# Kernel tuning notes

Measured on AMD Instinct MI355X. Metric: run time of the kernel, lower is better.

The kernel has to match this reference:

```python
import jax, jax.numpy as jnp
import numpy as np

H, W, CIN, COUT, B = 56, 56, 64, 64, 32
K = 3            # kernel_size
WIN = 15         # win_range
R = (WIN - 1) // 2


def _make_sample_idx():
    """Per-pixel fixed random sample locations within a WINxWIN window,
    mirroring Dconv_drop.__init__ (random.sample over valid window indices)."""
    rng = np.random.default_rng(0)
    ii = np.arange(H)[:, None, None]          # [H,1,1]
    jj = np.arange(W)[None, :, None]          # [1,W,1]
    lo_i = np.maximum(0, ii - R); hi_i = np.minimum(H - 1, ii + R)
    lo_j = np.maximum(0, jj - R); hi_j = np.minimum(W - 1, jj + R)
    ri = rng.integers(np.broadcast_to(lo_i, (H, W, K * K)),
                      np.broadcast_to(hi_i, (H, W, K * K)) + 1)
    rj = rng.integers(np.broadcast_to(lo_j, (H, W, K * K)),
                      np.broadcast_to(hi_j, (H, W, K * K)) + 1)
    return (ri * W + rj).astype(np.int32)    # [H,W,9] indices into H*W


def setup_inputs() -> dict:
    key = jax.random.key(0)
    k1, k2 = jax.random.split(key)
    x = jax.random.normal(k1, (B, CIN, H, W), dtype=jnp.float32)
    weight = jax.random.normal(k2, (COUT, CIN, K, K), dtype=jnp.float32) * 0.05
    sample_idx = jnp.asarray(_make_sample_idx())
    return {"x": x, "weight": weight, "sample_idx": sample_idx}


def reference(x, weight, sample_idx):
    # x: [B,C,H,W]; sample_idx: [H,W,9] flat indices into H*W.
    # Original: scatter gathered pixels into [B,C,3H,3W] grid, then
    # stride-3 kernel-3 conv => per-pixel contraction over the 9 samples.
    b, c, h, w = x.shape
    x_flat = x.reshape(b, c, h * w)
    gathered = x_flat[:, :, sample_idx]              # [B,C,H,W,9]
    w_flat = weight.reshape(weight.shape[0], c, K * K)  # [O,C,9]
    out = jnp.einsum('bchwk,ock->bohw', gathered, w_flat)
    return out
```

## Files before the change

kernel.cpp:

```cpp
#include <hip/hip_runtime.h>
#include <hip/hip_bf16.h>

#define HH 56
#define WW 56
#define CIN 64
#define COUT 64
#define BATCH 32
#define KK 9
#define HWP (HH*WW)
#define NS 18
#define NTILE 49
#define NBLK (NTILE*BATCH)
#define XT_OFF 73728
#define XSW 33

typedef __attribute__((ext_vector_type(8))) short short8;
typedef __attribute__((ext_vector_type(4))) float float4v;
typedef __attribute__((ext_vector_type(4))) unsigned int uint4v;

__device__ __forceinline__ unsigned short f2bf(float f) {
    union { float f; unsigned u; } v; v.f = f;
    unsigned r = v.u + 0x7FFFu + ((v.u >> 16) & 1u);
    return (unsigned short)(r >> 16);
}

__device__ __forceinline__ void prepack_elem(const float* __restrict__ w,
                                             unsigned short* __restrict__ apack,
                                             int e) {
    int j = e & 7;
    int l = (e >> 3) & 63;
    int ss = e >> 9;
    int mb = ss / 18;
    int s  = ss - mb * 18;
    int o = mb * 16 + (l & 15);
    int c = ((s & 1) << 5) + ((l >> 4) << 3) + j;
    int k = s >> 1;
    apack[e] = f2bf(w[(o * CIN + c) * KK + k]);
}

__global__ __launch_bounds__(256) void prep_kernel(
    const float* __restrict__ x, const float* __restrict__ w,
    unsigned int* __restrict__ xt, unsigned short* __restrict__ apack)
{
    int bid = blockIdx.x;
    int t   = threadIdx.x;
    if (bid < 784) {
        int u   = bid * 256 + t;
        int c2q = u & 7;
        int hq  = u >> 3;
        int b   = hq / 784;
        int q   = hq - b * 784;
        int hw  = q * 4;
        const float* xb = x + ((size_t)b * CIN + c2q * 8) * HWP + hw;
        float4v f[8];
        #pragma unroll
        for (int i = 0; i < 8; ++i)
            f[i] = *(const float4v*)(xb + (size_t)i * HWP);
        unsigned int* xto = xt + ((size_t)b * HWP + hw) * 32 + c2q * 4;
        #pragma unroll
        for (int j = 0; j < 4; ++j) {
            uint4v o;
            #pragma unroll
            for (int ci = 0; ci < 4; ++ci)
                o[ci] = (unsigned)f2bf(f[2 * ci][j]) |
                        ((unsigned)f2bf(f[2 * ci + 1][j]) << 16);
            *(uint4v*)(xto + (size_t)j * 32) = o;
        }
    } else {
        prepack_elem(w, apack, (bid - 784) * 256 + t);
    }
}

__global__ __launch_bounds__(256) void prep_weights_only(
    const float* __restrict__ w, unsigned short* __restrict__ apack)
{
    prepack_elem(w, apack, blockIdx.x * 256 + threadIdx.x);
}

__global__ __launch_bounds__(256) void dconv_main(
    const unsigned int* __restrict__ xt, const int* __restrict__ sidx,
    const unsigned short* __restrict__ apack, float* __restrict__ out)
{
    __shared__ unsigned int xs[496 * 16];

    const int t    = threadIdx.x;
    const int lane = t & 63;
    const int wv   = t >> 6;
    const int mbp  = wv >> 1;
    const int ntp  = wv & 1;
    const int col  = lane & 15;
    const int krow = lane >> 4;

    int bid  = blockIdx.x;
    int orig = (bid & 7) * 196 + (bid >> 3);
    int b    = orig / NTILE;
    int bx   = orig - b * NTILE;
    int ti = bx / 7, tj = bx - (bx / 7) * 7;
    int r0 = ti * 8 - 7; if (r0 < 0) r0 = 0;
    int c0 = tj * 8 - 7; if (c0 < 0) c0 = 0;

    const unsigned int* xtb = xt + (size_t)b * HWP * 32;

    int lb[2][KK];
    #pragma unroll
    for (int nn = 0; nn < 2; ++nn) {
        int p  = (ntp * 2 + nn) * 16 + col;
        int gi = ti * 8 + (p >> 3), gj = tj * 8 + (p & 7);
        const int* sp = sidx + (gi * WW + gj) * KK;
        #pragma unroll
        for (int k = 0; k < KK; ++k) {
            int g  = sp[k];
            int si = g / WW, sj = g - si * WW;
            int row = (si - r0) * 22 + (sj - c0);
            lb[nn][k] = row * 64 + ((krow ^ (row & 3)) << 4);
        }
    }

    const unsigned short* apW = apack + (size_t)(mbp * 2 * NS) * 512 + lane * 8;

    float4v zero = {0.f, 0.f, 0.f, 0.f};
    float4v acc[2][2] = {{zero, zero}, {zero, zero}};
    const char* xsb = (const char*)xs;

    #pragma unroll
    for (int sh = 0; sh < 2; ++sh) {
        for (int grp = wv; grp < 31; grp += 4) {
            int row = grp * 16 + (lane >> 2);
            int rc  = row < 483 ? row : 483;
            int lsr = rc / 22;
            int lsc = rc - lsr * 22;
            int si = r0 + lsr; if (si > HH - 1) si = HH - 1;
            int sj = c0 + lsc; if (sj > WW - 1) sj = WW - 1;
            int q  = (lane & 3) ^ (rc & 3);
            const unsigned int* src =
                xtb + (size_t)(si * WW + sj) * 32 + sh * 16 + (q << 2);
            __builtin_amdgcn_global_load_lds(
                (const __attribute__((address_space(1))) unsigned int*)src,
                (__attribute__((address_space(3))) unsigned int*)(xs + grp * 256),
                16, 0, 0);
        }
        __syncthreads();

        #pragma unroll
        for (int k = 0; k < KK; ++k) {
            short8 a0 = *(const short8*)(apW + (size_t)(2 * k + sh) * 512);
            short8 a1 = *(const short8*)(apW + (size_t)(NS + 2 * k + sh) * 512);
            #pragma unroll
            for (int nn = 0; nn < 2; ++nn) {
                short8 bv = *(const short8*)(xsb + lb[nn][k]);
                acc[0][nn] = __builtin_amdgcn_mfma_f32_16x16x32_bf16(
                    a0, bv, acc[0][nn], 0, 0, 0);
                acc[1][nn] = __builtin_amdgcn_mfma_f32_16x16x32_bf16(
                    a1, bv, acc[1][nn], 0, 0, 0);
            }
        }
        if (sh == 0) __syncthreads();
    }

    float* ob = out + ((size_t)b * COUT + mbp * 32) * HWP;
    #pragma unroll
    for (int m = 0; m < 2; ++m) {
        #pragma unroll
        for (int nn = 0; nn < 2; ++nn) {
            int p = (ntp * 2 + nn) * 16 + col;
            int g = (ti * 8 + (p >> 3)) * WW + tj * 8 + (p & 7);
            #pragma unroll
            for (int r = 0; r < 4; ++r)
                ob[(m * 16 + krow * 4 + r) * HWP + g] = acc[m][nn][r];
        }
    }
}

__global__ __launch_bounds__(256, 2) void dconv_fb(
    const float* __restrict__ x, const int* __restrict__ sidx,
    const unsigned short* __restrict__ apack, float* __restrict__ out)
{
    __shared__ unsigned int xs[484 * XSW];

    const int t    = threadIdx.x;
    const int lane = t & 63;
    const int wv   = t >> 6;
    const int mbp  = wv >> 1;
    const int ntp  = wv & 1;
    const int col  = lane & 15;
    const int krow = lane >> 4;
    const int bx   = blockIdx.x;
    const int b    = blockIdx.y;
    const int ti = bx / 7, tj = bx - (bx / 7) * 7;
    int r0 = ti * 8 - 7; if (r0 < 0) r0 = 0;
    int r1 = ti * 8 + 14; if (r1 > HH - 1) r1 = HH - 1;
    int c0 = tj * 8 - 7; if (c0 < 0) c0 = 0;
    int c1 = tj * 8 + 14; if (c1 > WW - 1) c1 = WW - 1;

    int lb[2][KK];
    #pragma unroll
    for (int nn = 0; nn < 2; ++nn) {
        int p  = (ntp * 2 + nn) * 16 + col;
        int gi = ti * 8 + (p >> 3), gj = tj * 8 + (p & 7);
        const int* sp = sidx + (gi * WW + gj) * KK;
        #pragma unroll
        for (int k = 0; k < KK; ++k) {
            int g  = sp[k];
            int si = g / WW, sj = g - si * WW;
            lb[nn][k] = ((si - r0) * 22 + (sj - c0)) * (XSW * 4);
        }
    }

    short8 areg[2][NS];
    #pragma unroll
    for (int m = 0; m < 2; ++m) {
        const unsigned short* ap = apack + ((mbp * 2 + m) * NS) * 512 + lane * 8;
        #pragma unroll
        for (int s = 0; s < NS; ++s)
            areg[m][s] = *(const short8*)(ap + s * 512);
    }

    const float* xb = x + (size_t)b * CIN * HWP;
    for (int e = t; e < 32 * 512; e += 256) {
        int c2 = e >> 9, ls = e & 511;
        if (ls < 484) {
            int lsr = ls / 22;
            int si = r0 + lsr, sj = c0 + (ls - lsr * 22);
            if (si <= r1 && sj <= c1) {
                int g = si * WW + sj;
                float f0 = xb[(2 * c2) * HWP + g];
                float f1 = xb[(2 * c2 + 1) * HWP + g];
                xs[ls * XSW + c2] =
                    (unsigned)f2bf(f0) | ((unsigned)f2bf(f1) << 16);
            }
        }
    }
    __syncthreads();

    float4v zero = {0.f, 0.f, 0.f, 0.f};
    float4v acc[2][2] = {{zero, zero}, {zero, zero}};
    const char* xsb = (const char*)xs + krow * 16;

    #pragma unroll
    for (int k = 0; k < KK; ++k) {
        #pragma unroll
        for (int nn = 0; nn < 2; ++nn) {
            const char* ba = xsb + lb[nn][k];
            union { int i[4]; short8 s8; } b0, b1;
            #pragma unroll
            for (int w = 0; w < 4; ++w) {
                b0.i[w] = *(const int*)(ba + w * 4);
                b1.i[w] = *(const int*)(ba + 64 + w * 4);
            }
            acc[0][nn] = __builtin_amdgcn_mfma_f32_16x16x32_bf16(
                areg[0][2 * k], b0.s8, acc[0][nn], 0, 0, 0);
            acc[1][nn] = __builtin_amdgcn_mfma_f32_16x16x32_bf16(
                areg[1][2 * k], b0.s8, acc[1][nn], 0, 0, 0);
            acc[0][nn] = __builtin_amdgcn_mfma_f32_16x16x32_bf16(
                areg[0][2 * k + 1], b1.s8, acc[0][nn], 0, 0, 0);
            acc[1][nn] = __builtin_amdgcn_mfma_f32_16x16x32_bf16(
                areg[1][2 * k + 1], b1.s8, acc[1][nn], 0, 0, 0);
        }
    }

    float* ob = out + ((size_t)b * COUT + mbp * 32) * HWP;
    #pragma unroll
    for (int m = 0; m < 2; ++m) {
        #pragma unroll
        for (int nn = 0; nn < 2; ++nn) {
            int p = (ntp * 2 + nn) * 16 + col;
            int g = (ti * 8 + (p >> 3)) * WW + tj * 8 + (p & 7);
            #pragma unroll
            for (int r = 0; r < 4; ++r)
                ob[(m * 16 + krow * 4 + r) * HWP + g] = acc[m][nn][r];
        }
    }
}

extern "C" void kernel_launch(void* const* d_in, const int* in_sizes, int n_in,
                              void* d_out, int out_size, void* d_ws, size_t ws_size,
                              hipStream_t stream) {
    const float* x    = (const float*)d_in[0];
    const float* w    = (const float*)d_in[1];
    const int*   sidx = (const int*)d_in[2];
    float* out = (float*)d_out;
    unsigned short* apack = (unsigned short*)d_ws;
    unsigned int*   xt    = (unsigned int*)((char*)d_ws + XT_OFF);

    size_t need = (size_t)XT_OFF + (size_t)BATCH * HWP * 128;
    if (ws_size >= need) {
        prep_kernel<<<928, 256, 0, stream>>>(x, w, xt, apack);
        dconv_main<<<NBLK, 256, 0, stream>>>(xt, sidx, apack, out);
    } else {
        prep_weights_only<<<144, 256, 0, stream>>>(w, apack);
        dim3 grid(NTILE, BATCH);
        dconv_fb<<<grid, 256, 0, stream>>>(x, sidx, apack, out);
    }
}
```

Before: 32.57 us.

## Enlarge output tile to 8x14 to cut halo overhead in main conv kernel

Changes the main kernel's spatial tile from 8x8 to 8x14 pixels, so 28 tiles per image replace 49, with a 22x28 staged input window instead of 22x22. Each wave now handles up to four 16-pixel column groups (4 or 3) rather than two, which amortises the halo load over more outputs and halves the block count. In exchange it uses more LDS and registers per block, has uneven work between the two wave halves, and launches fewer blocks.

```diff
diff --git a/kernel.cpp b/kernel.cpp
--- a/kernel.cpp
+++ b/kernel.cpp
@@ -9,10 +9,12 @@
 #define KK 9
 #define HWP (HH*WW)
 #define NS 18
-#define NTILE 49
+#define NTILE 28
 #define NBLK (NTILE*BATCH)
 #define XT_OFF 73728
 #define XSW 33
+#define RSTR 28
+#define NGRP 39
 
 typedef __attribute__((ext_vector_type(8))) short short8;
 typedef __attribute__((ext_vector_type(4))) float float4v;
@@ -81,54 +83,66 @@
     const unsigned int* __restrict__ xt, const int* __restrict__ sidx,
     const unsigned short* __restrict__ apack, float* __restrict__ out)
 {
-    __shared__ unsigned int xs[496 * 16];
+    __shared__ unsigned int xs[NGRP * 16 * 16];
 
     const int t    = threadIdx.x;
     const int lane = t & 63;
     const int wv   = t >> 6;
     const int mbp  = wv >> 1;
-    const int ntp  = wv & 1;
+    const int nh   = wv & 1;
+    const int nn0  = nh * 4;
+    const int nnc  = nh ? 3 : 4;
     const int col  = lane & 15;
     const int krow = lane >> 4;
 
     int bid  = blockIdx.x;
-    int orig = (bid & 7) * 196 + (bid >> 3);
+    int orig = (bid & 7) * 112 + (bid >> 3);
     int b    = orig / NTILE;
     int bx   = orig - b * NTILE;
-    int ti = bx / 7, tj = bx - (bx / 7) * 7;
-    int r0 = ti * 8 - 7; if (r0 < 0) r0 = 0;
-    int c0 = tj * 8 - 7; if (c0 < 0) c0 = 0;
+    int ti  = bx >> 2;
+    int tjj = bx & 3;
+    int r0 = ti * 8 - 7;   if (r0 < 0) r0 = 0;
+    int c0 = tjj * 14 - 7; if (c0 < 0) c0 = 0;
 
     const unsigned int* xtb = xt + (size_t)b * HWP * 32;
 
-    int lb[2][KK];
-    #pragma unroll
-    for (int nn = 0; nn < 2; ++nn) {
-        int p  = (ntp * 2 + nn) * 16 + col;
-        int gi = ti * 8 + (p >> 3), gj = tj * 8 + (p & 7);
-        const int* sp = sidx + (gi * WW + gj) * KK;
-        #pragma unroll
-        for (int k = 0; k < KK; ++k) {
-            int g  = sp[k];
-            int si = g / WW, sj = g - si * WW;
-            int row = (si - r0) * 22 + (sj - c0);
-            lb[nn][k] = row * 64 + ((krow ^ (row & 3)) << 4);
+    int lb[4][KK];
+    int gout[4];
+    #pragma unroll
+    for (int nn = 0; nn < 4; ++nn) {
+        if (nn < nnc) {
+            int p  = (nn0 + nn) * 16 + col;
+            int pr = p / 14, pc = p - pr * 14;
+            int gi = ti * 8 + pr, gj = tjj * 14 + pc;
+            gout[nn] = gi * WW + gj;
+            const int* sp = sidx + (gi * WW + gj) * KK;
+            #pragma unroll
+            for (int k = 0; k < KK; ++k) {
+                int g  = sp[k];
+                int si = g / WW, sj = g - si * WW;
+                int row = (si - r0) * RSTR + (sj - c0);
+                lb[nn][k] = row * 64 + ((krow ^ (row & 3)) << 4);
+            }
         }
     }
 
     const unsigned short* apW = apack + (size_t)(mbp * 2 * NS) * 512 + lane * 8;
 
     float4v zero = {0.f, 0.f, 0.f, 0.f};
-    float4v acc[2][2] = {{zero, zero}, {zero, zero}};
+    float4v acc[2][4];
+    #pragma unroll
+    for (int m = 0; m < 2; ++m)
+        #pragma unroll
+        for (int nn = 0; nn < 4; ++nn) acc[m][nn] = zero;
     const char* xsb = (const char*)xs;
 
     #pragma unroll
     for (int sh = 0; sh < 2; ++sh) {
-        for (int grp = wv; grp < 31; grp += 4) {
+        for (int grp = wv; grp < NGRP; grp += 4) {
             int row = grp * 16 + (lane >> 2);
-            int rc  = row < 483 ? row : 483;
-            int lsr = rc / 22;
-            int lsc = rc - lsr * 22;
+            int rc  = row < 615 ? row : 615;
+            int lsr = rc / RSTR;
+            int lsc = rc - lsr * RSTR;
             int si = r0 + lsr; if (si > HH - 1) si = HH - 1;
             int sj = c0 + lsc; if (sj > WW - 1) sj = WW - 1;
             int q  = (lane & 3) ^ (rc & 3);
@@ -146,12 +160,14 @@
             short8 a0 = *(const short8*)(apW + (size_t)(2 * k + sh) * 512);
             short8 a1 = *(const short8*)(apW + (size_t)(NS + 2 * k + sh) * 512);
             #pragma unroll
-            for (int nn = 0; nn < 2; ++nn) {
-                short8 bv = *(const short8*)(xsb + lb[nn][k]);
-                acc[0][nn] = __builtin_amdgcn_mfma_f32_16x16x32_bf16(
-                    a0, bv, acc[0][nn], 0, 0, 0);
-                acc[1][nn] = __builtin_amdgcn_mfma_f32_16x16x32_bf16(
-                    a1, bv, acc[1][nn], 0, 0, 0);
+            for (int nn = 0; nn < 4; ++nn) {
+                if (nn < nnc) {
+                    short8 bv = *(const short8*)(xsb + lb[nn][k]);
+                    acc[0][nn] = __builtin_amdgcn_mfma_f32_16x16x32_bf16(
+                        a0, bv, acc[0][nn], 0, 0, 0);
+                    acc[1][nn] = __builtin_amdgcn_mfma_f32_16x16x32_bf16(
+                        a1, bv, acc[1][nn], 0, 0, 0);
+                }
             }
         }
         if (sh == 0) __syncthreads();
@@ -161,12 +177,13 @@
     #pragma unroll
     for (int m = 0; m < 2; ++m) {
         #pragma unroll
-        for (int nn = 0; nn < 2; ++nn) {
-            int p = (ntp * 2 + nn) * 16 + col;
-            int g = (ti * 8 + (p >> 3)) * WW + tj * 8 + (p & 7);
-            #pragma unroll
-            for (int r = 0; r < 4; ++r)
-                ob[(m * 16 + krow * 4 + r) * HWP + g] = acc[m][nn][r];
+        for (int nn = 0; nn < 4; ++nn) {
+            if (nn < nnc) {
+                int g = gout[nn];
+                #pragma unroll
+                for (int r = 0; r < 4; ++r)
+                    ob[(m * 16 + krow * 4 + r) * HWP + g] = acc[m][nn][r];
+            }
         }
     }
 }
@@ -288,7 +305,7 @@
         dconv_main<<<NBLK, 256, 0, stream>>>(xt, sidx, apack, out);
     } else {
         prep_weights_only<<<144, 256, 0, stream>>>(w, apack);
-        dim3 grid(NTILE, BATCH);
+        dim3 grid(49, BATCH);
         dconv_fb<<<grid, 256, 0, stream>>>(x, sidx, apack, out);
     }
 }
```

Result: no change. 33.17 us (+1.8%).
